# Performance work log

Hardware: AMD Instinct MI355X
Metric: run time of the kernel (lower is better)

The kernel has to match this reference:

```python
import jax, jax.numpy as jnp
import numpy as np

N = 50000          # num nodes
E = 800000         # num edges
IN_F = 128
OUT_F = 64
H = 4
D = OUT_F // H     # head_dim = 16
EPS = 1e-9
ACOSH_EPS = 1e-6


def _minkowski(a, b):
    # Minkowski-style inner product used by ProjectiveUHG: +...+,- signature
    return jnp.sum(a[..., :-1] * b[..., :-1], axis=-1) - a[..., -1] * b[..., -1]


def _uhg_distance(a, b):
    # d = arccosh( sqrt( <a,b>^2 / (<a,a><b,b>) ) ), clamped for validity
    num = _minkowski(a, b) ** 2
    den = _minkowski(a, a) * _minkowski(b, b)
    ratio = num / jnp.maximum(jnp.abs(den), EPS)
    return jnp.arccosh(jnp.maximum(jnp.sqrt(ratio + EPS), 1.0 + ACOSH_EPS))


def setup_inputs() -> dict:
    key = jax.random.key(0)
    ks = jax.random.split(key, 12)
    s_in = 1.0 / np.sqrt(IN_F)
    s_out = 1.0 / np.sqrt(OUT_F)
    return {
        "x": jax.random.normal(ks[0], (N, IN_F), dtype=jnp.float32),
        "edge_index": jax.random.randint(ks[1], (2, E), 0, N, dtype=jnp.int64),
        "Wq": jax.random.normal(ks[2], (OUT_F, IN_F), dtype=jnp.float32) * s_in,
        "bq": jax.random.normal(ks[3], (OUT_F,), dtype=jnp.float32) * s_in,
        "Wk": jax.random.normal(ks[4], (OUT_F, IN_F), dtype=jnp.float32) * s_in,
        "bk": jax.random.normal(ks[5], (OUT_F,), dtype=jnp.float32) * s_in,
        "Wv": jax.random.normal(ks[6], (OUT_F, IN_F), dtype=jnp.float32) * s_in,
        "bv": jax.random.normal(ks[7], (OUT_F,), dtype=jnp.float32) * s_in,
        "Wo": jax.random.normal(ks[8], (OUT_F, OUT_F), dtype=jnp.float32) * s_out,
        "bo": jax.random.normal(ks[9], (OUT_F,), dtype=jnp.float32) * s_out,
    }


def reference(x, edge_index, Wq, bq, Wk, bk, Wv, bv, Wo, bo):
    n = x.shape[0]
    q = (x @ Wq.T + bq).reshape(n, H, D)
    k = (x @ Wk.T + bk).reshape(n, H, D)
    v = (x @ Wv.T + bv).reshape(n, H, D)

    src = edge_index[0]
    dst = edge_index[1]

    # per-edge, per-head hyperbolic distance scores  [E, H]
    qe = q[src]                      # [E, H, D]
    ke = k[dst]                      # [E, H, D]
    scores = -_uhg_distance(qe, ke)  # [E, H]

    # per-destination-node softmax over incoming edges (stable)
    smax = jax.ops.segment_max(scores, dst, num_segments=n)  # [N, H]
    ex = jnp.exp(scores - smax[dst])
    denom = jax.ops.segment_sum(ex, dst, num_segments=n)     # [N, H]
    w = ex / jnp.maximum(denom[dst], EPS)                    # [E, H]

    # weighted scatter-aggregate of source values, then projective average
    # (weighted sum normalized to unit L2 norm per head)
    agg = jax.ops.segment_sum(w[..., None] * v[src], dst, num_segments=n)  # [N, H, D]
    norm = jnp.linalg.norm(agg, axis=-1, keepdims=True)
    attended = agg / (norm + EPS)  # isolated nodes stay zero

    out = attended.reshape(n, OUT_F) @ Wo.T + bo
    return out  # dropout is identity in eval mode
```

## Files before the change

### kernel.cpp

```cpp
#include <hip/hip_runtime.h>
#include <hip/hip_fp16.h>

#define NNODES 50000
#define NEDGES 800000
#define IN_FEAT 128
#define OUT_FEAT 64
#define NH 4
#define HD 16

#define XS_P 132
#define WS_P 196
#define CAP 96

__global__ void detect_kernel(const void* __restrict__ ei, int* __restrict__ flag) {
    const unsigned long long* p = (const unsigned long long*)ei;
    unsigned long long v = p[threadIdx.x];
    if (v >> 32) atomicOr(flag, 1);
}

__device__ __forceinline__ float r16(float x) {
    x += __shfl_xor(x, 1, 16);
    x += __shfl_xor(x, 2, 16);
    x += __shfl_xor(x, 4, 16);
    x += __shfl_xor(x, 8, 16);
    return x;
}

__device__ __forceinline__ float r4(float x) {
    x += __shfl_xor(x, 1, 4);
    x += __shfl_xor(x, 2, 4);
    return x;
}

__global__ __launch_bounds__(256) void qkv_kernel(
        const float* __restrict__ x,
        const float* __restrict__ Wq, const float* __restrict__ bq,
        const float* __restrict__ Wk, const float* __restrict__ bk,
        const float* __restrict__ Wv, const float* __restrict__ bv,
        __half2* __restrict__ qv2, float* __restrict__ ktn) {
    __shared__ float xs[64 * XS_P];
    __shared__ float ws[16 * WS_P];
    const int tid = threadIdx.x;
    const int nb = blockIdx.x * 64;
    const int tx = tid & 15;
    const int ty = tid >> 4;

#pragma unroll
    for (int j = 0; j < 8; ++j) {
        int f4 = tid + j * 256;
        int r = f4 >> 5, c = (f4 & 31) * 4;
        int n = nb + r; if (n >= NNODES) n = NNODES - 1;
        float4 vx = *(const float4*)(x + (size_t)n * IN_FEAT + c);
        *(float4*)(xs + r * XS_P + c) = vx;
    }

    float acc[4][12];
#pragma unroll
    for (int ii = 0; ii < 4; ++ii)
#pragma unroll
        for (int jj = 0; jj < 12; ++jj) acc[ii][jj] = 0.0f;

    for (int ch = 0; ch < 8; ++ch) {
        __syncthreads();
#pragma unroll
        for (int jj = 0; jj < 12; ++jj) {
            int i = tid + jj * 256;
            int r = i >> 4, kk = i & 15;
            const float* W = (r < 64) ? Wq : (r < 128) ? Wk : Wv;
            ws[kk * WS_P + r] = W[(r & 63) * IN_FEAT + ch * 16 + kk];
        }
        __syncthreads();
#pragma unroll
        for (int kk = 0; kk < 16; ++kk) {
            int k = ch * 16 + kk;
            float4 wq4 = *(const float4*)(ws + kk * WS_P + tx * 4);
            float4 wk4 = *(const float4*)(ws + kk * WS_P + 64 + tx * 4);
            float4 wv4 = *(const float4*)(ws + kk * WS_P + 128 + tx * 4);
            float xv[4];
#pragma unroll
            for (int ii = 0; ii < 4; ++ii) xv[ii] = xs[(ty + 16 * ii) * XS_P + k];
#pragma unroll
            for (int ii = 0; ii < 4; ++ii) {
                acc[ii][0] = fmaf(xv[ii], wq4.x, acc[ii][0]);
                acc[ii][1] = fmaf(xv[ii], wq4.y, acc[ii][1]);
                acc[ii][2] = fmaf(xv[ii], wq4.z, acc[ii][2]);
                acc[ii][3] = fmaf(xv[ii], wq4.w, acc[ii][3]);
                acc[ii][4] = fmaf(xv[ii], wk4.x, acc[ii][4]);
                acc[ii][5] = fmaf(xv[ii], wk4.y, acc[ii][5]);
                acc[ii][6] = fmaf(xv[ii], wk4.z, acc[ii][6]);
                acc[ii][7] = fmaf(xv[ii], wk4.w, acc[ii][7]);
                acc[ii][8]  = fmaf(xv[ii], wv4.x, acc[ii][8]);
                acc[ii][9]  = fmaf(xv[ii], wv4.y, acc[ii][9]);
                acc[ii][10] = fmaf(xv[ii], wv4.z, acc[ii][10]);
                acc[ii][11] = fmaf(xv[ii], wv4.w, acc[ii][11]);
            }
        }
    }

    float bqr[4], bkr[4], bvr[4];
#pragma unroll
    for (int j = 0; j < 4; ++j) {
        bqr[j] = bq[tx * 4 + j];
        bkr[j] = bk[tx * 4 + j];
        bvr[j] = bv[tx * 4 + j];
    }
    const float slast = ((tx & 3) == 3) ? -1.0f : 1.0f;

#pragma unroll
    for (int ii = 0; ii < 4; ++ii) {
        int n = nb + ty + 16 * ii;
        float qr[4], kr[4], vr[4];
#pragma unroll
        for (int j = 0; j < 4; ++j) {
            qr[j] = acc[ii][j] + bqr[j];
            kr[j] = acc[ii][4 + j] + bkr[j];
            vr[j] = acc[ii][8 + j] + bvr[j];
        }
        float lq = qr[0]*qr[0] + qr[1]*qr[1] + qr[2]*qr[2] + slast * qr[3]*qr[3];
        float lk = kr[0]*kr[0] + kr[1]*kr[1] + kr[2]*kr[2] + slast * kr[3]*kr[3];
        float aa = r4(lq);
        float bb = r4(lk);
        float rsa = __builtin_amdgcn_rsqf(fmaxf(fabsf(aa), 1e-12f));
        float rsb = __builtin_amdgcn_rsqf(fmaxf(fabsf(bb), 1e-12f));
        float kn[4];
        __half2 h[4];
#pragma unroll
        for (int j = 0; j < 4; ++j) {
            h[j] = __floats2half2_rn(qr[j] * rsa, vr[j]);
            kn[j] = kr[j] * rsb;
        }
        kn[3] *= slast;
        if (n < NNODES) {
            *(float4*)(qv2 + (size_t)n * 64 + tx * 4) = *(float4*)h;
            *(float4*)(ktn + (size_t)n * 64 + tx * 4) = make_float4(kn[0], kn[1], kn[2], kn[3]);
        }
    }
}

__global__ void build_kernel(const void* __restrict__ ei, const int* __restrict__ mode,
                             int* __restrict__ deg, int* __restrict__ ssrc) {
    int e = blockIdx.x * blockDim.x + threadIdx.x;
    if (e >= NEDGES) return;
    int si, di;
    if (*mode) {
        const int* p = (const int*)ei;
        si = p[e]; di = p[NEDGES + e];
    } else {
        const long long* p = (const long long*)ei;
        si = (int)p[e]; di = (int)p[NEDGES + e];
    }
    int pos = atomicAdd(&deg[di], 1);
    if (pos < CAP) ssrc[di * CAP + pos] = si;
}

__global__ __launch_bounds__(256) void agg_kernel(
        const int* __restrict__ deg, const int* __restrict__ ssrc,
        const __half2* __restrict__ qv2, const float* __restrict__ ktn,
        const float* __restrict__ Wo, const float* __restrict__ bo,
        float* __restrict__ out) {
    __shared__ float atts[256];
    const int tid = threadIdx.x;
    const int n = blockIdx.x * 4 + (tid >> 6);
    const int t = tid & 63;

    const float kt = ktn[n * 64 + t];

    int cnt_all = deg[n]; if (cnt_all > CAP) cnt_all = CAP;
    const int base0 = n * CAP;
    float acc = 0.0f, den = 0.0f;
    for (int base = 0; base < cnt_all; base += 64) {
        int cnt = cnt_all - base; if (cnt > 64) cnt = 64;
        int sv = (t < cnt) ? ssrc[base0 + base + t] : 0;
        int j = 0;
        for (; j + 3 < cnt; j += 4) {
            int s0 = __shfl(sv, j, 64);
            int s1 = __shfl(sv, j + 1, 64);
            int s2 = __shfl(sv, j + 2, 64);
            int s3 = __shfl(sv, j + 3, 64);
            float2 f0 = __half22float2(qv2[(size_t)s0 * 64 + t]);
            float2 f1 = __half22float2(qv2[(size_t)s1 * 64 + t]);
            float2 f2 = __half22float2(qv2[(size_t)s2 * 64 + t]);
            float2 f3 = __half22float2(qv2[(size_t)s3 * 64 + t]);
            float ab0 = r16(f0.x * kt);
            float ab1 = r16(f1.x * kt);
            float ab2 = r16(f2.x * kt);
            float ab3 = r16(f3.x * kt);
            float x0 = fmaxf(fabsf(ab0), 1.0f + 1e-6f);
            float x1 = fmaxf(fabsf(ab1), 1.0f + 1e-6f);
            float x2 = fmaxf(fabsf(ab2), 1.0f + 1e-6f);
            float x3 = fmaxf(fabsf(ab3), 1.0f + 1e-6f);
            float e0 = __builtin_amdgcn_rcpf(x0 + sqrtf(fmaf(x0, x0, -1.0f)));
            float e1 = __builtin_amdgcn_rcpf(x1 + sqrtf(fmaf(x1, x1, -1.0f)));
            float e2 = __builtin_amdgcn_rcpf(x2 + sqrtf(fmaf(x2, x2, -1.0f)));
            float e3 = __builtin_amdgcn_rcpf(x3 + sqrtf(fmaf(x3, x3, -1.0f)));
            acc = fmaf(e0, f0.y, acc); den += e0;
            acc = fmaf(e1, f1.y, acc); den += e1;
            acc = fmaf(e2, f2.y, acc); den += e2;
            acc = fmaf(e3, f3.y, acc); den += e3;
        }
        for (; j < cnt; ++j) {
            int s0 = __shfl(sv, j, 64);
            float2 f0 = __half22float2(qv2[(size_t)s0 * 64 + t]);
            float ab0 = r16(f0.x * kt);
            float x0 = fmaxf(fabsf(ab0), 1.0f + 1e-6f);
            float e0 = __builtin_amdgcn_rcpf(x0 + sqrtf(fmaf(x0, x0, -1.0f)));
            acc = fmaf(e0, f0.y, acc); den += e0;
        }
    }

    float ss = r16(acc * acc);
    float att = 0.0f;
    if (ss > 0.0f) att = acc / (sqrtf(ss) + 1e-9f * den);
    atts[tid] = att;
    __syncthreads();

    const float4* av = (const float4*)(atts + (tid & 192));
    const float4* wr = (const float4*)(Wo + t * 64);
    float o = 0.0f;
#pragma unroll
    for (int j = 0; j < 16; ++j) {
        float4 w = wr[j], a = av[j];
        o += a.x * w.x + a.y * w.y + a.z * w.z + a.w * w.w;
    }
    out[n * 64 + t] = o + bo[t];
}

extern "C" void kernel_launch(void* const* d_in, const int* in_sizes, int n_in,
                              void* d_out, int out_size, void* d_ws, size_t ws_size,
                              hipStream_t stream) {
    const float* x  = (const float*)d_in[0];
    const void*  ei = d_in[1];
    const float* Wq = (const float*)d_in[2];
    const float* bq = (const float*)d_in[3];
    const float* Wk = (const float*)d_in[4];
    const float* bk = (const float*)d_in[5];
    const float* Wv = (const float*)d_in[6];
    const float* bv = (const float*)d_in[7];
    const float* Wo = (const float*)d_in[8];
    const float* bo = (const float*)d_in[9];
    float* out = (float*)d_out;

    __half2* qv2  = (__half2*)d_ws;
    float* ktn    = (float*)(qv2 + (size_t)NNODES * 64);
    int*   deg    = (int*)(ktn + (size_t)NNODES * 64);
    int*   flg    = deg + NNODES;
    int*   ssrc   = flg + 1;

    hipMemsetAsync(deg, 0, (size_t)(NNODES + 1) * sizeof(int), stream);

    detect_kernel<<<1, 256, 0, stream>>>(ei, flg);
    qkv_kernel<<<(NNODES + 63) / 64, 256, 0, stream>>>(x, Wq, bq, Wk, bk, Wv, bv, qv2, ktn);
    build_kernel<<<(NEDGES + 255) / 256, 256, 0, stream>>>(ei, flg, deg, ssrc);
    agg_kernel<<<NNODES / 4, 256, 0, stream>>>(deg, ssrc, qv2, ktn, Wo, bo, out);
}
```

Baseline: 302.7 us.

## Assign one edge per lane with per-lane head-dot, then transpose-reduce accumulators

The aggregation kernel is remapped so that each of the 16 lanes in a head group handles a different incoming edge. Each lane loads that edge's full 16-dim q/v slice as float4s and computes the dot product locally, so the per-edge 16-lane shuffle reduction goes away. The 16-element per-lane accumulators are then combined with a butterfly transpose-reduce at the end. This uses more registers, and lanes sit idle when the degree is not a multiple of 16.

New measurement: 337.1 us. 1.11x slower.

```diff
diff --git a/kernel.cpp b/kernel.cpp
--- a/kernel.cpp
+++ b/kernel.cpp
@@ -162,55 +162,91 @@
     const int tid = threadIdx.x;
     const int n = blockIdx.x * 4 + (tid >> 6);
     const int t = tid & 63;
-
-    const float kt = ktn[n * 64 + t];
-
-    int cnt_all = deg[n]; if (cnt_all > CAP) cnt_all = CAP;
+    const int h = t >> 4;
+    const int es = t & 15;
+
+    float kf[16];
+    {
+        const float4* kp = (const float4*)(ktn + n * 64 + h * 16);
+        float4 k0 = kp[0], k1 = kp[1], k2 = kp[2], k3 = kp[3];
+        kf[0]=k0.x; kf[1]=k0.y; kf[2]=k0.z; kf[3]=k0.w;
+        kf[4]=k1.x; kf[5]=k1.y; kf[6]=k1.z; kf[7]=k1.w;
+        kf[8]=k2.x; kf[9]=k2.y; kf[10]=k2.z; kf[11]=k2.w;
+        kf[12]=k3.x; kf[13]=k3.y; kf[14]=k3.z; kf[15]=k3.w;
+    }
+
+    int cnt = deg[n]; if (cnt > CAP) cnt = CAP;
     const int base0 = n * CAP;
-    float acc = 0.0f, den = 0.0f;
-    for (int base = 0; base < cnt_all; base += 64) {
-        int cnt = cnt_all - base; if (cnt > 64) cnt = 64;
-        int sv = (t < cnt) ? ssrc[base0 + base + t] : 0;
-        int j = 0;
-        for (; j + 3 < cnt; j += 4) {
-            int s0 = __shfl(sv, j, 64);
-            int s1 = __shfl(sv, j + 1, 64);
-            int s2 = __shfl(sv, j + 2, 64);
-            int s3 = __shfl(sv, j + 3, 64);
-            float2 f0 = __half22float2(qv2[(size_t)s0 * 64 + t]);
-            float2 f1 = __half22float2(qv2[(size_t)s1 * 64 + t]);
-            float2 f2 = __half22float2(qv2[(size_t)s2 * 64 + t]);
-            float2 f3 = __half22float2(qv2[(size_t)s3 * 64 + t]);
-            float ab0 = r16(f0.x * kt);
-            float ab1 = r16(f1.x * kt);
-            float ab2 = r16(f2.x * kt);
-            float ab3 = r16(f3.x * kt);
-            float x0 = fmaxf(fabsf(ab0), 1.0f + 1e-6f);
-            float x1 = fmaxf(fabsf(ab1), 1.0f + 1e-6f);
-            float x2 = fmaxf(fabsf(ab2), 1.0f + 1e-6f);
-            float x3 = fmaxf(fabsf(ab3), 1.0f + 1e-6f);
-            float e0 = __builtin_amdgcn_rcpf(x0 + sqrtf(fmaf(x0, x0, -1.0f)));
-            float e1 = __builtin_amdgcn_rcpf(x1 + sqrtf(fmaf(x1, x1, -1.0f)));
-            float e2 = __builtin_amdgcn_rcpf(x2 + sqrtf(fmaf(x2, x2, -1.0f)));
-            float e3 = __builtin_amdgcn_rcpf(x3 + sqrtf(fmaf(x3, x3, -1.0f)));
-            acc = fmaf(e0, f0.y, acc); den += e0;
-            acc = fmaf(e1, f1.y, acc); den += e1;
-            acc = fmaf(e2, f2.y, acc); den += e2;
-            acc = fmaf(e3, f3.y, acc); den += e3;
-        }
-        for (; j < cnt; ++j) {
-            int s0 = __shfl(sv, j, 64);
-            float2 f0 = __half22float2(qv2[(size_t)s0 * 64 + t]);
-            float ab0 = r16(f0.x * kt);
-            float x0 = fmaxf(fabsf(ab0), 1.0f + 1e-6f);
-            float e0 = __builtin_amdgcn_rcpf(x0 + sqrtf(fmaf(x0, x0, -1.0f)));
-            acc = fmaf(e0, f0.y, acc); den += e0;
-        }
-    }
-
-    float ss = r16(acc * acc);
+    const float4* qp = (const float4*)qv2;
+
+    float acc[16];
+#pragma unroll
+    for (int d = 0; d < 16; ++d) acc[d] = 0.0f;
+    float den = 0.0f;
+
+    for (int base = 0; base < cnt; base += 16) {
+        int idx = base + es;
+        bool on = idx < cnt;
+        int sv = on ? ssrc[base0 + idx] : 0;
+        int q4 = sv * 16 + h * 4;
+        float4 A = qp[q4], B = qp[q4 + 1], C = qp[q4 + 2], D = qp[q4 + 3];
+        float qd[16], vd[16];
+        {
+            const __half2* pa = (const __half2*)&A;
+            const __half2* pb = (const __half2*)&B;
+            const __half2* pc = (const __half2*)&C;
+            const __half2* pd = (const __half2*)&D;
+#pragma unroll
+            for (int j = 0; j < 4; ++j) {
+                float2 fa = __half22float2(pa[j]); qd[j]      = fa.x; vd[j]      = fa.y;
+                float2 fb = __half22float2(pb[j]); qd[4 + j]  = fb.x; vd[4 + j]  = fb.y;
+                float2 fc = __half22float2(pc[j]); qd[8 + j]  = fc.x; vd[8 + j]  = fc.y;
+                float2 fd = __half22float2(pd[j]); qd[12 + j] = fd.x; vd[12 + j] = fd.y;
+            }
+        }
+        float d0 = 0.0f, d1 = 0.0f, d2 = 0.0f, d3 = 0.0f;
+#pragma unroll
+        for (int j = 0; j < 4; ++j) {
+            d0 = fmaf(qd[j],      kf[j],      d0);
+            d1 = fmaf(qd[4 + j],  kf[4 + j],  d1);
+            d2 = fmaf(qd[8 + j],  kf[8 + j],  d2);
+            d3 = fmaf(qd[12 + j], kf[12 + j], d3);
+        }
+        float dot = (d0 + d1) + (d2 + d3);
+        float xv = fmaxf(fabsf(dot), 1.0f + 1e-6f);
+        float ex = __builtin_amdgcn_rcpf(xv + sqrtf(fmaf(xv, xv, -1.0f)));
+        ex = on ? ex : 0.0f;
+        den += ex;
+#pragma unroll
+        for (int d = 0; d < 16; ++d) acc[d] = fmaf(ex, vd[d], acc[d]);
+    }
+
+    float den_t = r16(den);
+
+    {
+        float t8[8], n8[8];
+#pragma unroll
+        for (int j = 0; j < 8; ++j) t8[j] = (es & 8) ? acc[j] : acc[j + 8];
+#pragma unroll
+        for (int j = 0; j < 8; ++j) n8[j] = ((es & 8) ? acc[j + 8] : acc[j]) + __shfl_xor(t8[j], 8, 16);
+        float t4[4], n4[4];
+#pragma unroll
+        for (int j = 0; j < 4; ++j) t4[j] = (es & 4) ? n8[j] : n8[j + 4];
+#pragma unroll
+        for (int j = 0; j < 4; ++j) n4[j] = ((es & 4) ? n8[j + 4] : n8[j]) + __shfl_xor(t4[j], 4, 16);
+        float t2[2], n2[2];
+#pragma unroll
+        for (int j = 0; j < 2; ++j) t2[j] = (es & 2) ? n4[j] : n4[j + 2];
+#pragma unroll
+        for (int j = 0; j < 2; ++j) n2[j] = ((es & 2) ? n4[j + 2] : n4[j]) + __shfl_xor(t2[j], 2, 16);
+        float t1 = (es & 1) ? n2[0] : n2[1];
+        acc[0] = ((es & 1) ? n2[1] : n2[0]) + __shfl_xor(t1, 1, 16);
+    }
+    float a0 = acc[0];
+
+    float ss = r16(a0 * a0);
     float att = 0.0f;
-    if (ss > 0.0f) att = acc / (sqrtf(ss) + 1e-9f * den);
+    if (ss > 0.0f) att = a0 / (sqrtf(ss) + 1e-9f * den_t);
     atts[tid] = att;
     __syncthreads();
 
```
